# Kernel tuning notes

Measured on AMD Instinct MI355X. Metric: run time of the kernel, lower is better.

Reference implementation:

```python
import jax, jax.numpy as jnp
import numpy as np

N_HEAD = 6


def setup_inputs() -> dict:
    key = jax.random.key(0)
    k1, k2, k3 = jax.random.split(key, 3)
    B, N, D = 16, 512, 768
    d_head = D // N_HEAD
    p_mask = jnp.ones((B, N), dtype=jnp.float32)
    feature = jax.random.normal(k1, (B, N, D), dtype=jnp.float32)
    # nn.Linear weights (out, in); scaled like torch default init
    W = jax.random.normal(k2, (D, D), dtype=jnp.float32) / np.sqrt(D)
    # attn Linear(2*d_head -> n_head); only the diagonal head rows are used
    Wa = jax.random.normal(k3, (N_HEAD, 2 * d_head), dtype=jnp.float32) / np.sqrt(2 * d_head)
    return {"p_mask": p_mask, "feature": feature, "W": W, "Wa": Wa, "num_layers": 2}


def reference(p_mask, feature, W, Wa, num_layers):
    B, N, D = feature.shape
    H = N_HEAD
    Dh = D // H
    # adj[b,q,k] = p_mask[b,q] * p_mask[b,k]  (bmm of unsqueezed mask)
    adj = p_mask[:, :, None] * p_mask[:, None, :]  # (B,N,N)
    mask = adj[:, :, :, None] > 0                   # (B,N,N,1)
    for _ in range(num_layers):
        residual = feature
        qk = (feature @ W.T).reshape(B, N, H, Dh)  # (B,N,H,Dh)
        # concat(q,k) @ Wa[h] decomposes into query part + key part
        sq = jnp.einsum('bqhd,hd->bqh', qk, Wa[:, :Dh])
        sk = jnp.einsum('bkhd,hd->bkh', qk, Wa[:, Dh:])
        score = jnp.tanh(sq[:, :, None, :] + sk[:, None, :, :])  # (B,N,N,H)
        # masked_fill with -1e-8 where adj == 0 (faithful to source)
        score = jnp.where(mask, score, jnp.float32(-1e-8))
        attn = jax.nn.softmax(score, axis=2)  # softmax over key dim (dim=-2)
        # dropout p=0 in eval -> identity
        hid = jnp.tanh(jnp.einsum('bqkh,bkhd->bqhd', attn, qk))  # (B,N,H,Dh)
        feature = residual + hid.reshape(B, N, D)
    return feature
```

## Files before the change

kernel.cpp:

```cpp
#include <hip/hip_runtime.h>
#include <hip/hip_bf16.h>
#include <stdint.h>

#define BATCH 16
#define NSEQ  512
#define DMODEL 768
#define NHEAD 6
#define DHEAD 128
#define MROWS (BATCH * NSEQ)
#define QBLK  32
#define KTILE 64

typedef __attribute__((ext_vector_type(8))) __bf16 bf16x8;
typedef __attribute__((ext_vector_type(4))) __bf16 bf16x4;
typedef __attribute__((ext_vector_type(4))) float  f32x4;
typedef __attribute__((ext_vector_type(4))) unsigned int u32x4;

#define GLD16(gp, lp) __builtin_amdgcn_global_load_lds( \
    (const __attribute__((address_space(1))) unsigned int*)(gp), \
    (__attribute__((address_space(3))) unsigned int*)(lp), 16, 0, 0)

#define BAR_PLAIN() do { asm volatile("" ::: "memory"); \
    __builtin_amdgcn_s_barrier(); asm volatile("" ::: "memory"); } while (0)
#define BAR_LGKM() do { asm volatile("s_waitcnt lgkmcnt(0)" ::: "memory"); \
    __builtin_amdgcn_s_barrier(); asm volatile("" ::: "memory"); } while (0)

__global__ void cvt_bf16_kernel(const float* __restrict__ src,
                                __bf16* __restrict__ dst, int n4) {
    int i = blockIdx.x * blockDim.x + threadIdx.x;
    if (i < n4) {
        float4 v = reinterpret_cast<const float4*>(src)[i];
        bf16x4 o;
        o.x = (__bf16)v.x; o.y = (__bf16)v.y; o.z = (__bf16)v.z; o.w = (__bf16)v.w;
        reinterpret_cast<bf16x4*>(dst)[i] = o;
    }
}

template<bool AFP32>
__global__ __launch_bounds__(256) void gemm_bt(const void* __restrict__ Av,
                                               const __bf16* __restrict__ Bm,
                                               __bf16* __restrict__ C,
                                               const float* __restrict__ Wa,
                                               const float* __restrict__ pmask,
                                               float* __restrict__ eq_t,
                                               float* __restrict__ ek_t) {
    const __bf16* Ab = reinterpret_cast<const __bf16*>(Av);
    const float*  Af = reinterpret_cast<const float*>(Av);

    __shared__ __align__(16) __bf16 As[2][AFP32 ? 4096 : 2048];
    __shared__ __align__(16) __bf16 Bs[2][128 * 32];
    const int tid  = threadIdx.x;
    const int lane = tid & 63;
    const int wave = tid >> 6;
    const int wm = wave >> 1, wn = wave & 1;

    const int wg  = blockIdx.x;
    const int nid = (wg & 7) * 96 + (wg >> 3);
    const int bx  = nid % 6;
    const int by  = nid / 6;
    const int m0 = by * 64;
    const int n0 = bx * 128;

    f32x4 acc[2][4] = {};

    const int e0   = tid * 8;
    const int row0 = tid >> 2;
    const int k0i  = (tid & 3) * 8;

    const int lr = lane & 15;
    const int lg = lane >> 4;
    const int kb = lg * 8;

    auto STAGE = [&](int kt, int bufi) {
        if constexpr (AFP32) {
            #pragma unroll
            for (int i2 = 0; i2 < 2; i2++) {
                int tt  = tid + 256 * i2;
                int row = tt >> 3;
                int k0s = ((tt & 7) * 4) ^ ((row & 7) << 2);
                GLD16(Af + (size_t)(m0 + row) * DMODEL + kt + k0s,
                      reinterpret_cast<float*>(&As[bufi][0]) + tt * 4);
            }
        } else {
            GLD16(Ab + (size_t)(m0 + row0) * DMODEL + kt + k0i, &As[bufi][e0]);
        }
        GLD16(Bm + (size_t)(n0 + row0)      * DMODEL + kt + k0i, &Bs[bufi][e0]);
        GLD16(Bm + (size_t)(n0 + row0 + 64) * DMODEL + kt + k0i, &Bs[bufi][e0 + 2048]);
    };

    STAGE(0, 0);

    for (int t = 0; t < 24; t++) {
        const int buf = t & 1;
        if (t < 23) {
            STAGE((t + 1) * 32, buf ^ 1);
            if constexpr (AFP32) asm volatile("s_waitcnt vmcnt(4)" ::: "memory");
            else                 asm volatile("s_waitcnt vmcnt(3)" ::: "memory");
        } else {
            asm volatile("s_waitcnt vmcnt(0)" ::: "memory");
        }
        __builtin_amdgcn_s_barrier();
        asm volatile("" ::: "memory");

        bf16x8 af[2], bfv[4];
        if constexpr (AFP32) {
            const float* A32 = reinterpret_cast<const float*>(&As[buf][0]);
            const int sw = (lr & 7) << 2;
            #pragma unroll
            for (int i = 0; i < 2; i++) {
                int row = wm * 32 + i * 16 + lr;
                f32x4 lo = *reinterpret_cast<const f32x4*>(&A32[row * 32 + (kb ^ sw)]);
                f32x4 hi = *reinterpret_cast<const f32x4*>(&A32[row * 32 + ((kb + 4) ^ sw)]);
                #pragma unroll
                for (int j = 0; j < 4; j++) {
                    af[i][j]     = (__bf16)lo[j];
                    af[i][4 + j] = (__bf16)hi[j];
                }
            }
        } else {
            #pragma unroll
            for (int i = 0; i < 2; i++)
                af[i] = *reinterpret_cast<const bf16x8*>(&As[buf][(wm * 32 + i * 16 + lr) * 32 + kb]);
        }
        #pragma unroll
        for (int j = 0; j < 4; j++)
            bfv[j] = *reinterpret_cast<const bf16x8*>(&Bs[buf][(wn * 64 + j * 16 + lr) * 32 + kb]);
        #pragma unroll
        for (int i = 0; i < 2; i++)
            #pragma unroll
            for (int j = 0; j < 4; j++)
                acc[i][j] = __builtin_amdgcn_mfma_f32_16x16x32_bf16(af[i], bfv[j], acc[i][j], 0, 0, 0);

        BAR_PLAIN();
    }

    const int rg = lg * 4;
    #pragma unroll
    for (int i = 0; i < 2; i++) {
        #pragma unroll
        for (int j = 0; j < 4; j++) {
            #pragma unroll
            for (int r = 0; r < 4; r++) {
                int row = m0 + wm * 32 + i * 16 + rg + r;
                int col = n0 + wn * 64 + j * 16 + lr;
                C[(size_t)row * DMODEL + col] = (__bf16)acc[i][j][r];
            }
        }
    }

    const int h = bx;
    float wqv[4], wkv[4];
    #pragma unroll
    for (int j = 0; j < 4; j++) {
        int d = wn * 64 + j * 16 + lr;
        wqv[j] = Wa[h * 256 + d];
        wkv[j] = Wa[h * 256 + 128 + d];
    }
    float* red = reinterpret_cast<float*>(&As[0][0]);
    #pragma unroll
    for (int i = 0; i < 2; i++) {
        #pragma unroll
        for (int r = 0; r < 4; r++) {
            float aq = 0.f, ak = 0.f;
            #pragma unroll
            for (int j = 0; j < 4; j++) {
                aq += acc[i][j][r] * wqv[j];
                ak += acc[i][j][r] * wkv[j];
            }
            #pragma unroll
            for (int off = 1; off < 16; off <<= 1) {
                aq += __shfl_xor(aq, off);
                ak += __shfl_xor(ak, off);
            }
            if (lr == 0) {
                int row = wm * 32 + i * 16 + rg + r;
                red[(0 * 64 + row) * 2 + wn] = aq;
                red[(1 * 64 + row) * 2 + wn] = ak;
            }
        }
    }
    __syncthreads();
    if (tid < 64) {
        int row = m0 + tid;
        float s = red[tid * 2] + red[tid * 2 + 1];
        eq_t[(size_t)h * MROWS + row] = (pmask[row] > 0.f) ? __expf(2.f * s) : 0.f;
    } else if (tid < 128) {
        int rl  = tid - 64;
        int row = m0 + rl;
        float s = red[(64 + rl) * 2] + red[(64 + rl) * 2 + 1];
        ek_t[(size_t)h * MROWS + row] = (pmask[row] > 0.f) ? __expf(2.f * s) : 0.f;
    }
}

template<int LAYER>
__global__ __launch_bounds__(256) void attn_pv(const __bf16* __restrict__ QK,
                                               const float* __restrict__ eq_t,
                                               const float* __restrict__ ek_t,
                                               const float* __restrict__ resf,
                                               const __bf16* __restrict__ resb,
                                               float* __restrict__ outf,
                                               __bf16* __restrict__ outb) {
    const int wg  = blockIdx.x;
    const int nid = (wg & 7) * 192 + (wg >> 3);
    const int qt = nid & 15;
    const int hb = nid >> 4;
    const int h  = hb % NHEAD;
    const int b  = hb / NHEAD;
    const int q0 = qt * QBLK;

    __shared__ __align__(16) __bf16 w[QBLK][512];
    __shared__ __align__(16) __bf16 Vt[2][DHEAD * KTILE];
    const int tid  = threadIdx.x;
    const int lane = tid & 63;
    const int wave = tid >> 6;

    const int wd0 = wave * 32;
    const int lr  = lane & 15;
    const int lg  = lane >> 4;

    const int sd0 = (tid & 15) * 8;
    const int sk0 = (tid >> 4) * 4;
    const __bf16* Vbase = QK + (size_t)b * NSEQ * DMODEL + (size_t)h * DHEAD + sd0;

    u32x4 A0, A1, A2, A3, B0, B1, B2, B3;
    #define LOADS(S0, S1, S2, S3, t) do { \
        const __bf16* p = Vbase + (size_t)((t) * KTILE + sk0) * DMODEL; \
        S0 = *reinterpret_cast<const u32x4*>(p); \
        S1 = *reinterpret_cast<const u32x4*>(p + DMODEL); \
        S2 = *reinterpret_cast<const u32x4*>(p + 2 * DMODEL); \
        S3 = *reinterpret_cast<const u32x4*>(p + 3 * DMODEL); \
    } while (0)
    #define WRITEV(S0, S1, S2, S3, bufi) do { \
        char* vtw = reinterpret_cast<char*>(&Vt[bufi][0]); \
        _Pragma("unroll") \
        for (int j = 0; j < 8; j++) { \
            int d = sd0 + j; \
            int swz = j ^ (tid & 7); \
            unsigned sel = (j & 1) ? 0x07060302u : 0x05040100u; \
            unsigned lo = __builtin_amdgcn_perm(S1[j >> 1], S0[j >> 1], sel); \
            unsigned hi = __builtin_amdgcn_perm(S3[j >> 1], S2[j >> 1], sel); \
            unsigned long long pk = (unsigned long long)lo | ((unsigned long long)hi << 32); \
            *reinterpret_cast<unsigned long long*>(vtw + d * 128 + ((sk0 ^ (swz << 3)) * 2)) = pk; \
        } \
    } while (0)

    LOADS(A0, A1, A2, A3, 0);
    LOADS(B0, B1, B2, B3, 1);

    float res[2][4][2];
    #pragma unroll
    for (int qh = 0; qh < 2; qh++) {
        #pragma unroll
        for (int r = 0; r < 4; r++) {
            int ql = qh * 16 + lg * 4 + r;
            #pragma unroll
            for (int n = 0; n < 2; n++) {
                int d = wd0 + n * 16 + lr;
                size_t o = ((size_t)(b * NSEQ + q0 + ql)) * DMODEL + (size_t)h * DHEAD + d;
                if constexpr (LAYER == 0) res[qh][r][n] = resf[o];
                else                      res[qh][r][n] = (float)resb[o];
            }
        }
    }

    const int k0 = lane * 8;
    const size_t sbase = (size_t)h * MROWS + b * NSEQ;
    float4 e0v = *reinterpret_cast<const float4*>(&ek_t[sbase + k0]);
    float4 e1v = *reinterpret_cast<const float4*>(&ek_t[sbase + k0 + 4]);
    float ek[8] = {e0v.x, e0v.y, e0v.z, e0v.w, e1v.x, e1v.y, e1v.z, e1v.w};
    float eq[8];
    #pragma unroll
    for (int g = 0; g < 8; g++)
        eq[g] = eq_t[sbase + q0 + wave * 8 + g];

    WRITEV(A0, A1, A2, A3, 0);
    LOADS(A0, A1, A2, A3, 2);

    #pragma unroll
    for (int g = 0; g < 8; g++) {
        int q = wave * 8 + g;
        float eqv = eq[g];
        bf16x8 wv;
        #pragma unroll
        for (int j = 0; j < 8; j++) {
            float u = eqv * ek[j];
            float z = __builtin_amdgcn_rcpf(u + 1.f);
            float p = __expf(fmaf(z, -2.f, 1.f));
            wv[j] = (__bf16)(u > 0.f ? p : 1.0f);
        }
        *reinterpret_cast<bf16x8*>(&w[q][k0 ^ ((q & 7) << 3)]) = wv;
    }
    BAR_LGKM();

    bf16x8 vones;
    #pragma unroll
    for (int e = 0; e < 8; e++) vones[e] = (__bf16)1.0f;

    f32x4 acc[2][2] = {};
    f32x4 accs[2] = {};

    const int wswz = (lr & 7) << 3;

    #pragma unroll
    for (int t = 0; t < 8; t++) {
        const int buf = t & 1;
        const char* vtr = reinterpret_cast<const char*>(&Vt[buf][0]);
        __builtin_amdgcn_s_setprio(1);
        #pragma unroll
        for (int ks = 0; ks < 2; ks++) {
            int cb = (t * 64 + ks * 32 + lg * 8) ^ wswz;
            bf16x8 af0 = *reinterpret_cast<const bf16x8*>(&w[lr][cb]);
            bf16x8 af1 = *reinterpret_cast<const bf16x8*>(&w[16 + lr][cb]);
            #pragma unroll
            for (int n = 0; n < 2; n++) {
                int d    = wd0 + n * 16 + lr;
                int kbk  = ks * 4 + lg;
                int swzd = (d & 7) ^ ((d >> 3) & 7);
                bf16x8 bv = *reinterpret_cast<const bf16x8*>(vtr + d * 128 + ((kbk ^ swzd) << 4));
                acc[0][n] = __builtin_amdgcn_mfma_f32_16x16x32_bf16(af0, bv, acc[0][n], 0, 0, 0);
                acc[1][n] = __builtin_amdgcn_mfma_f32_16x16x32_bf16(af1, bv, acc[1][n], 0, 0, 0);
            }
            accs[0] = __builtin_amdgcn_mfma_f32_16x16x32_bf16(af0, vones, accs[0], 0, 0, 0);
            accs[1] = __builtin_amdgcn_mfma_f32_16x16x32_bf16(af1, vones, accs[1], 0, 0, 0);
        }
        __builtin_amdgcn_s_setprio(0);
        if (t < 7) {
            if ((t & 1) == 0) WRITEV(B0, B1, B2, B3, buf ^ 1);
            else              WRITEV(A0, A1, A2, A3, buf ^ 1);
        }
        if (t < 5) {
            if ((t & 1) == 0) LOADS(B0, B1, B2, B3, t + 3);
            else              LOADS(A0, A1, A2, A3, t + 3);
        }
        if (t < 7) BAR_LGKM();
    }

    #pragma unroll
    for (int qh = 0; qh < 2; qh++) {
        #pragma unroll
        for (int r = 0; r < 4; r++) {
            int ql = qh * 16 + lg * 4 + r;
            float rden = __builtin_amdgcn_rcpf(accs[qh][r]);
            #pragma unroll
            for (int n = 0; n < 2; n++) {
                int d  = wd0 + n * 16 + lr;
                float hv = acc[qh][n][r] * rden;
                float e2 = __expf(2.f * hv);
                float tv = 1.f - 2.f * __builtin_amdgcn_rcpf(e2 + 1.f);
                size_t o = ((size_t)(b * NSEQ + q0 + ql)) * DMODEL + (size_t)h * DHEAD + d;
                float ov = res[qh][r][n] + tv;
                if constexpr (LAYER == 0) outb[o] = (__bf16)ov;
                else                      outf[o] = ov;
            }
        }
    }
    #undef LOADS
    #undef WRITEV
}

extern "C" void kernel_launch(void* const* d_in, const int* in_sizes, int n_in,
                              void* d_out, int out_size, void* d_ws, size_t ws_size,
                              hipStream_t stream) {
    const float* pmask   = (const float*)d_in[0];
    const float* feature = (const float*)d_in[1];
    const float* W       = (const float*)d_in[2];
    const float* Wa      = (const float*)d_in[3];
    float* out = (float*)d_out;
    char* ws = (char*)d_ws;

    __bf16* Abf  = (__bf16*)ws;
    __bf16* Wbf  = (__bf16*)(ws + 12582912);
    __bf16* QKbf = (__bf16*)(ws + 12582912 + 1179648);
    float*  eq   = (float*)(ws + 12582912 + 1179648 + 12582912);
    float*  ek   = eq + MROWS * NHEAD;

    const int wN4 = (DMODEL * DMODEL) / 4;

    hipLaunchKernelGGL(cvt_bf16_kernel, dim3((wN4 + 255) / 256), dim3(256), 0, stream,
                       W, Wbf, wN4);

    hipLaunchKernelGGL((gemm_bt<true>), dim3(768), dim3(256), 0, stream,
                       (const void*)feature, Wbf, QKbf, Wa, pmask, eq, ek);
    hipLaunchKernelGGL((attn_pv<0>), dim3(1536), dim3(256), 0, stream,
                       QKbf, eq, ek, feature, (const __bf16*)nullptr,
                       (float*)nullptr, Abf);

    hipLaunchKernelGGL((gemm_bt<false>), dim3(768), dim3(256), 0, stream,
                       (const void*)Abf, Wbf, QKbf, Wa, pmask, eq, ek);
    hipLaunchKernelGGL((attn_pv<1>), dim3(1536), dim3(256), 0, stream,
                       QKbf, eq, ek, (const float*)nullptr, Abf,
                       out, (__bf16*)nullptr);
}
```

Measured before the change: 103.7 us.

## Give each wave a private V-transpose slice to drop per-tile block barriers

The V tile staging in LDS is repartitioned so each wave loads, transposes and stores only the 32 head-dim columns it consumes. Each wave gets its own single-buffered slice instead of a shared double buffer. This removes the workgroup-wide barrier after every K tile and replaces it with a local lgkmcnt wait before overwriting the slice. Waves can drift independently, which trades the barrier cost for reduced cross-wave overlap and single buffering within a wave.

```diff
diff --git a/kernel.cpp b/kernel.cpp
--- a/kernel.cpp
+++ b/kernel.cpp
@@ -209,7 +209,7 @@
     const int q0 = qt * QBLK;
 
     __shared__ __align__(16) __bf16 w[QBLK][512];
-    __shared__ __align__(16) __bf16 Vt[2][DHEAD * KTILE];
+    __shared__ __align__(16) __bf16 Vt[4][32 * KTILE];
     const int tid  = threadIdx.x;
     const int lane = tid & 63;
     const int wave = tid >> 6;
@@ -218,29 +218,29 @@
     const int lr  = lane & 15;
     const int lg  = lane >> 4;
 
-    const int sd0 = (tid & 15) * 8;
-    const int sk0 = (tid >> 4) * 4;
-    const __bf16* Vbase = QK + (size_t)b * NSEQ * DMODEL + (size_t)h * DHEAD + sd0;
+    const int kg = lane >> 2;
+    const int dg = lane & 3;
+    const __bf16* Vbase = QK + (size_t)b * NSEQ * DMODEL + (size_t)h * DHEAD + wd0 + dg * 8;
+    char* vtw = reinterpret_cast<char*>(&Vt[0][0]) + wave * 4096;
 
     u32x4 A0, A1, A2, A3, B0, B1, B2, B3;
     #define LOADS(S0, S1, S2, S3, t) do { \
-        const __bf16* p = Vbase + (size_t)((t) * KTILE + sk0) * DMODEL; \
+        const __bf16* p = Vbase + (size_t)((t) * KTILE + kg * 4) * DMODEL; \
         S0 = *reinterpret_cast<const u32x4*>(p); \
         S1 = *reinterpret_cast<const u32x4*>(p + DMODEL); \
         S2 = *reinterpret_cast<const u32x4*>(p + 2 * DMODEL); \
         S3 = *reinterpret_cast<const u32x4*>(p + 3 * DMODEL); \
     } while (0)
-    #define WRITEV(S0, S1, S2, S3, bufi) do { \
-        char* vtw = reinterpret_cast<char*>(&Vt[bufi][0]); \
+    #define WRITEV(S0, S1, S2, S3) do { \
         _Pragma("unroll") \
         for (int j = 0; j < 8; j++) { \
-            int d = sd0 + j; \
-            int swz = j ^ (tid & 7); \
+            int dl = dg * 8 + j; \
+            int sw = j ^ dg; \
             unsigned sel = (j & 1) ? 0x07060302u : 0x05040100u; \
             unsigned lo = __builtin_amdgcn_perm(S1[j >> 1], S0[j >> 1], sel); \
             unsigned hi = __builtin_amdgcn_perm(S3[j >> 1], S2[j >> 1], sel); \
             unsigned long long pk = (unsigned long long)lo | ((unsigned long long)hi << 32); \
-            *reinterpret_cast<unsigned long long*>(vtw + d * 128 + ((sk0 ^ (swz << 3)) * 2)) = pk; \
+            *reinterpret_cast<unsigned long long*>(vtw + dl * 128 + (((kg * 4) ^ (sw << 3)) * 2)) = pk; \
         } \
     } while (0)
 
@@ -273,7 +273,7 @@
     for (int g = 0; g < 8; g++)
         eq[g] = eq_t[sbase + q0 + wave * 8 + g];
 
-    WRITEV(A0, A1, A2, A3, 0);
+    WRITEV(A0, A1, A2, A3);
     LOADS(A0, A1, A2, A3, 2);
 
     #pragma unroll
@@ -303,8 +303,6 @@
 
     #pragma unroll
     for (int t = 0; t < 8; t++) {
-        const int buf = t & 1;
-        const char* vtr = reinterpret_cast<const char*>(&Vt[buf][0]);
         __builtin_amdgcn_s_setprio(1);
         #pragma unroll
         for (int ks = 0; ks < 2; ks++) {
@@ -313,10 +311,10 @@
             bf16x8 af1 = *reinterpret_cast<const bf16x8*>(&w[16 + lr][cb]);
             #pragma unroll
             for (int n = 0; n < 2; n++) {
-                int d    = wd0 + n * 16 + lr;
-                int kbk  = ks * 4 + lg;
-                int swzd = (d & 7) ^ ((d >> 3) & 7);
-                bf16x8 bv = *reinterpret_cast<const bf16x8*>(vtr + d * 128 + ((kbk ^ swzd) << 4));
+                int dl   = n * 16 + lr;
+                int sw   = (dl & 7) ^ ((dl >> 3) & 7);
+                bf16x8 bv = *reinterpret_cast<const bf16x8*>(
+                    vtw + dl * 128 + (((ks * 4 + lg) ^ sw) << 4));
                 acc[0][n] = __builtin_amdgcn_mfma_f32_16x16x32_bf16(af0, bv, acc[0][n], 0, 0, 0);
                 acc[1][n] = __builtin_amdgcn_mfma_f32_16x16x32_bf16(af1, bv, acc[1][n], 0, 0, 0);
             }
@@ -325,14 +323,15 @@
         }
         __builtin_amdgcn_s_setprio(0);
         if (t < 7) {
-            if ((t & 1) == 0) WRITEV(B0, B1, B2, B3, buf ^ 1);
-            else              WRITEV(A0, A1, A2, A3, buf ^ 1);
+            __builtin_amdgcn_sched_barrier(0);
+            asm volatile("s_waitcnt lgkmcnt(0)" ::: "memory");
+            if ((t & 1) == 0) WRITEV(B0, B1, B2, B3);
+            else              WRITEV(A0, A1, A2, A3);
         }
         if (t < 5) {
             if ((t & 1) == 0) LOADS(B0, B1, B2, B3, t + 3);
             else              LOADS(A0, A1, A2, A3, t + 3);
         }
-        if (t < 7) BAR_LGKM();
     }
 
     #pragma unroll
```

New measurement: 99.16 us, median of 2. 1.05x faster.
